# Kernel tuning notes

Measured on AMD Instinct MI355X. Metric: run time of the kernel, lower is better.

The kernel has to match this reference:

```python
import jax, jax.numpy as jnp
import numpy as np

K = 1024
D = 256
BETA = 0.25


def setup_inputs() -> dict:
    key = jax.random.key(0)
    kx, kc = jax.random.split(key)
    x = jax.random.normal(kx, (64, 32, 32, D), dtype=jnp.float32)
    limit = 1.0 / K
    codebook = jax.random.uniform(kc, (K, D), dtype=jnp.float32, minval=-limit, maxval=limit)
    return {"x": x, "codebook": codebook}


def reference(x, codebook):
    flat = x.reshape(-1, D)                                   # [N, D]
    x2 = jnp.sum(jnp.square(flat), axis=1, keepdims=True)     # [N, 1]
    e2 = jnp.sum(jnp.square(codebook), axis=1)                # [K]
    sim = flat @ codebook.T                                   # [N, K]
    dist = x2 + e2 - 2.0 * sim                                # [N, K]
    idx = jnp.argmin(dist, axis=1)                            # [N]
    q = codebook[idx].reshape(x.shape)                        # [..., D]

    q_st = jax.lax.stop_gradient(q)
    x_st = jax.lax.stop_gradient(x)
    commit = jnp.mean(jnp.square(q_st - x))
    codebk = jnp.mean(jnp.square(q - x_st))
    loss = BETA * commit + codebk

    # code-usage statistics via histogram (equivalent to mean of one-hot)
    counts = jnp.zeros((K,), dtype=x.dtype).at[idx].add(1.0)
    probs = counts / flat.shape[0]
    eps = jnp.asarray(1e-10, dtype=x.dtype)
    H = -jnp.sum(probs * jnp.log2(probs + eps))               # bits/index
    perplexity = jnp.exp(H * jnp.log(jnp.asarray(2.0, dtype=x.dtype)))
    usage = jnp.sum((probs > 0).astype(x.dtype)) / float(K)

    y = x + jax.lax.stop_gradient(q - x)                      # straight-through
    return y, idx, loss, perplexity, usage, H
```

## Files before the change

### kernel.cpp

```cpp
#include <hip/hip_runtime.h>
#include <math.h>

#define D       256
#define KCODES  1024
#define NROWS   65536
#define BETA    0.25f
#define MARGIN  1e-3f
#define MAXSURV 7

typedef __attribute__((ext_vector_type(8))) short bf16x8;
typedef __attribute__((ext_vector_type(4))) float f32x4;

__device__ __forceinline__ unsigned int bf16_rne(float f) {
    unsigned int u = __float_as_uint(f);
    return (u + 0x7FFFu + ((u >> 16) & 1u)) >> 16;
}
__device__ __forceinline__ f32x4 mfma16(bf16x8 a, bf16x8 b, f32x4 c) {
    return __builtin_amdgcn_mfma_f32_16x16x32_bf16(a, b, c, 0, 0, 0);
}

__global__ __launch_bounds__(256) void split_cb_kernel(const float* __restrict__ cb,
                                                       ushort* __restrict__ cs,
                                                       float* __restrict__ e2f) {
    int code = blockIdx.x * 4 + (threadIdx.x >> 6);
    int lane = threadIdx.x & 63;
    float4 v = ((const float4*)(cb + (size_t)code * D))[lane];
    double s = (double)v.x * v.x + (double)v.y * v.y +
               (double)v.z * v.z + (double)v.w * v.w;
    ushort* ph = cs + (size_t)code * 256 + lane * 4;
    ph[0] = (ushort)bf16_rne(v.x); ph[1] = (ushort)bf16_rne(v.y);
    ph[2] = (ushort)bf16_rne(v.z); ph[3] = (ushort)bf16_rne(v.w);
    #pragma unroll
    for (int off = 32; off > 0; off >>= 1) s += __shfl_down(s, off, 64);
    if (lane == 0) e2f[code] = (float)s;
}

__global__ __launch_bounds__(256, 1) void screen_kernel(
    const float* __restrict__ x, const ushort* __restrict__ cs,
    const float* __restrict__ e2f, float* __restrict__ x2f,
    ushort* __restrict__ rowlist)
{
    __shared__ __attribute__((aligned(16))) ushort Bt[2][32 * 264];
    unsigned* mrg = (unsigned*)&Bt[0][0];
    #define MRG(r, j) mrg[(r) * 33 + (j)]

    const int tid  = threadIdx.x;
    const int wave = tid >> 6, lane = tid & 63;
    const int quad = lane >> 4, m = lane & 15;
    const int rowBase = blockIdx.x * 256;
    const int wrb = rowBase + wave * 64;

    const int sc = tid & 31, sp = tid >> 5;
    bf16x8 stg[4];
    {
        const ushort* src = cs + (size_t)sc * 256 + sp * 32;
        #pragma unroll
        for (int i = 0; i < 4; ++i) stg[i] = *(const bf16x8*)&src[i * 8];
    }

    bf16x8 af[4][8];
    #pragma unroll
    for (int t = 0; t < 4; ++t) {
        const float* xr = x + (size_t)(wrb + t * 16 + m) * D;
        double s = 0.0;
        #pragma unroll
        for (int c = 0; c < 8; ++c) {
            float4 f0 = *(const float4*)&xr[c * 32 + quad * 8];
            float4 f1 = *(const float4*)&xr[c * 32 + quad * 8 + 4];
            s += (double)f0.x * f0.x + (double)f0.y * f0.y +
                 (double)f0.z * f0.z + (double)f0.w * f0.w;
            s += (double)f1.x * f1.x + (double)f1.y * f1.y +
                 (double)f1.z * f1.z + (double)f1.w * f1.w;
            float ff[8] = {f0.x, f0.y, f0.z, f0.w, f1.x, f1.y, f1.z, f1.w};
            #pragma unroll
            for (int j = 0; j < 8; ++j) af[t][c][j] = (short)bf16_rne(ff[j]);
        }
        s += __shfl_xor(s, 16, 64);
        s += __shfl_xor(s, 32, 64);
        if (quad == 0) x2f[wrb + t * 16 + m] = (float)s;
    }

    unsigned u1[4][4], u2[4][4];
    #pragma unroll
    for (int t = 0; t < 4; ++t)
        #pragma unroll
        for (int r = 0; r < 4; ++r) { u1[t][r] = 0xFFFFFFFFu; u2[t][r] = 0xFFFFFFFFu; }

    for (int kt = 0; kt < KCODES / 32; ++kt) {
        {
            ushort* dst = &Bt[kt & 1][sc * 264 + sp * 32];
            #pragma unroll
            for (int i = 0; i < 4; ++i) *(bf16x8*)&dst[i * 8] = stg[i];
        }
        __syncthreads();
        if (kt < KCODES / 32 - 1) {
            const ushort* src = cs + (size_t)((kt + 1) * 32 + sc) * 256 + sp * 32;
            #pragma unroll
            for (int i = 0; i < 4; ++i) stg[i] = *(const bf16x8*)&src[i * 8];
        }

        float e2pa = e2f[kt * 32 + m] + 0.5f;
        float e2pb = e2f[kt * 32 + 16 + m] + 0.5f;

        const ushort* Bcur = &Bt[kt & 1][0];
        #pragma unroll
        for (int nt = 0; nt < 2; ++nt) {
            f32x4 acc0 = {0.f, 0.f, 0.f, 0.f};
            f32x4 acc1 = {0.f, 0.f, 0.f, 0.f};
            f32x4 acc2 = {0.f, 0.f, 0.f, 0.f};
            f32x4 acc3 = {0.f, 0.f, 0.f, 0.f};
            const ushort* bp = Bcur + (nt * 16 + m) * 264 + quad * 8;
            __builtin_amdgcn_s_setprio(1);
            #pragma unroll
            for (int c = 0; c < 8; ++c) {
                bf16x8 bh = *(const bf16x8*)&bp[c * 32];
                acc0 = mfma16(af[0][c], bh, acc0);
                acc1 = mfma16(af[1][c], bh, acc1);
                acc2 = mfma16(af[2][c], bh, acc2);
                acc3 = mfma16(af[3][c], bh, acc3);
            }
            __builtin_amdgcn_s_setprio(0);
            unsigned kcode = kt * 32 + nt * 16 + m;
            float e2p = nt ? e2pb : e2pa;
            #pragma unroll
            for (int t = 0; t < 4; ++t) {
                f32x4 acc = (t == 0) ? acc0 : (t == 1) ? acc1 : (t == 2) ? acc2 : acc3;
                #pragma unroll
                for (int r = 0; r < 4; ++r) {
                    float d = fmaf(-2.f, acc[r], e2p);
                    unsigned u = (__float_as_uint(d) & 0xFFFFFC00u) | kcode;
                    bool lt1 = u < u1[t][r];
                    bool lt2 = u < u2[t][r];
                    u2[t][r] = lt2 ? (lt1 ? u1[t][r] : u) : u2[t][r];
                    u1[t][r] = lt1 ? u : u1[t][r];
                }
            }
        }
    }

    #pragma unroll
    for (int ph = 0; ph < 2; ++ph) {
        if ((wave >> 1) == ph) {
            #pragma unroll
            for (int t = 0; t < 4; ++t)
                #pragma unroll
                for (int r = 0; r < 4; ++r) {
                    int rowloc = (wave & 1) * 64 + t * 16 + quad * 4 + r;
                    MRG(rowloc, m * 2 + 0) = u1[t][r];
                    MRG(rowloc, m * 2 + 1) = u2[t][r];
                }
        }
        __syncthreads();
        if (tid < 128) {
            unsigned umin = 0xFFFFFFFFu;
            #pragma unroll
            for (int j = 0; j < 32; ++j) umin = min(umin, MRG(tid, j));
            float dfloor = __uint_as_float(umin & 0xFFFFFC00u);
            unsigned limu = (__float_as_uint(dfloor + MARGIN) & 0xFFFFFC00u) | 1023u;
            ushort out[8] = {0, 0, 0, 0, 0, 0, 0, 0};
            int cnt = 0;
            for (int j = 0; j < 32; ++j) {
                unsigned u = MRG(tid, j);
                if (u <= limu && cnt < MAXSURV) { out[1 + cnt] = (ushort)(u & 1023u); ++cnt; }
            }
            out[0] = (ushort)cnt;
            *(bf16x8*)&rowlist[(size_t)(rowBase + ph * 128 + tid) * 8] = *(bf16x8*)out;
        }
        __syncthreads();
    }
    #undef MRG
}

__global__ __launch_bounds__(256) void rescore_kernel(
    const float* __restrict__ x, const float* __restrict__ cb,
    const float* __restrict__ x2f, const float* __restrict__ e2f,
    const ushort* __restrict__ rowlist, float* __restrict__ out_idxf,
    unsigned int* __restrict__ counts, float* __restrict__ y,
    float* __restrict__ msepart)
{
    int row  = blockIdx.x * 4 + (threadIdx.x >> 6);
    int lane = threadIdx.x & 63;
    const ushort* lst = rowlist + (size_t)row * 8;
    int cnt = lst[0];
    float4 xv = ((const float4*)(x + (size_t)row * D))[lane];

    int bk;
    if (cnt == 1) {
        bk = lst[1];
    } else {
        float x2 = x2f[row];
        float bestd = 1e30f;
        int   bestk = 0;
        for (int s = 0; s < cnt; ++s) {
            int k = lst[1 + s];
            float4 cv = ((const float4*)(cb + (size_t)k * D))[lane];
            double p = (double)xv.x * cv.x + (double)xv.y * cv.y +
                       (double)xv.z * cv.z + (double)xv.w * cv.w;
            #pragma unroll
            for (int off = 32; off > 0; off >>= 1) p += __shfl_down(p, off, 64);
            float simf = (float)p;
            float tt   = x2 + e2f[k];
            float dq   = tt - 2.0f * simf;
            if (dq < bestd || (dq == bestd && k < bestk)) { bestd = dq; bestk = k; }
        }
        bk = __shfl(bestk, 0, 64);
    }
    if (lane == 0) {
        out_idxf[row] = (float)bk;
        atomicAdd(&counts[bk], 1u);
    }
    float4 q = ((const float4*)(cb + (size_t)bk * D))[lane];
    float4 dv;
    dv.x = q.x - xv.x; dv.y = q.y - xv.y; dv.z = q.z - xv.z; dv.w = q.w - xv.w;
    float4 yv;
    yv.x = xv.x + dv.x; yv.y = xv.y + dv.y; yv.z = xv.z + dv.z; yv.w = xv.w + dv.w;
    ((float4*)(y + (size_t)row * D))[lane] = yv;
    float s = dv.x * dv.x + dv.y * dv.y + dv.z * dv.z + dv.w * dv.w;
    #pragma unroll
    for (int off = 32; off > 0; off >>= 1) s += __shfl_down(s, off, 64);
    if (lane == 0) msepart[row] = s;
}

__global__ __launch_bounds__(1024) void stats_kernel(
    const unsigned int* __restrict__ counts, const float* __restrict__ msepart,
    float* __restrict__ outs)
{
    int t = threadIdx.x;
    float ms = 0.f;
    #pragma unroll
    for (int j = 0; j < 64; ++j) ms += msepart[t + 1024 * j];

    float p = (float)counts[t] * (1.0f / 65536.0f);
    float h = -p * log2f(p + 1e-10f);
    float u = (p > 0.f) ? 1.f : 0.f;
    #pragma unroll
    for (int off = 32; off > 0; off >>= 1) {
        h  += __shfl_down(h,  off, 64);
        u  += __shfl_down(u,  off, 64);
        ms += __shfl_down(ms, off, 64);
    }
    __shared__ float hs[16], us[16], mss[16];
    int lane = t & 63, w = t >> 6;
    if (lane == 0) { hs[w] = h; us[w] = u; mss[w] = ms; }
    __syncthreads();
    if (t == 0) {
        float H = 0.f, U = 0.f, M = 0.f;
        #pragma unroll
        for (int i = 0; i < 16; ++i) { H += hs[i]; U += us[i]; M += mss[i]; }
        float m = M * (1.0f / 16777216.0f);
        float loss = BETA * m + m;
        float perp = expf(H * 0.69314718055994530942f);
        outs[0] = loss;
        outs[1] = perp;
        outs[2] = U * (1.0f / 1024.0f);
        outs[3] = H;
    }
}

extern "C" void kernel_launch(void* const* d_in, const int* in_sizes, int n_in,
                              void* d_out, int out_size, void* d_ws, size_t ws_size,
                              hipStream_t stream) {
    const float* x  = (const float*)d_in[0];
    const float* cb = (const float*)d_in[1];
    float* out      = (float*)d_out;

    float* y        = out;
    float* out_idxf = out + 16777216;
    float* outs     = out + 16777216 + 65536;

    float*        x2f     = (float*)d_ws;
    float*        e2f     = (float*)((char*)d_ws + 262144);
    unsigned int* counts  = (unsigned int*)((char*)d_ws + 266240);
    ushort*       rowlist = (ushort*)((char*)d_ws + 270400);
    ushort*       cs      = (ushort*)((char*)d_ws + 1318976);
    float*        msepart = (float*)((char*)d_ws + 1843264);

    hipMemsetAsync((char*)d_ws + 266240, 0, 4096, stream);
    split_cb_kernel<<<KCODES / 4, 256, 0, stream>>>(cb, cs, e2f);
    screen_kernel<<<NROWS / 256, 256, 0, stream>>>(x, cs, e2f, x2f, rowlist);
    rescore_kernel<<<NROWS / 4, 256, 0, stream>>>(x, cb, x2f, e2f, rowlist,
                                                  out_idxf, counts, y, msepart);
    stats_kernel<<<1, 1024, 0, stream>>>(counts, msepart, outs);
}
```

Before: 221.5 us.

## Restructure screen kernel to 8 waves of 16 rows each for higher occupancy

The screen kernel changes from 256-thread blocks where each wave handles 64 rows (four 16-row MFMA tiles) to 512-thread blocks of 128 rows where each wave handles a single 16-row tile. Per-thread register use (A fragments, accumulators, top-2 trackers) drops about fourfold, so launch bounds allow up to four blocks per CU instead of one. The aim is more waves in flight to hide latency. In exchange, each codebook tile staged into LDS is reused across 4x fewer rows per wave, which raises LDS read traffic per MFMA and adds more barrier participants.

```diff
diff --git a/kernel.cpp b/kernel.cpp
--- a/kernel.cpp
+++ b/kernel.cpp
@@ -35,7 +35,7 @@
     if (lane == 0) e2f[code] = (float)s;
 }
 
-__global__ __launch_bounds__(256, 1) void screen_kernel(
+__global__ __launch_bounds__(512, 4) void screen_kernel(
     const float* __restrict__ x, const ushort* __restrict__ cs,
     const float* __restrict__ e2f, float* __restrict__ x2f,
     ushort* __restrict__ rowlist)
@@ -47,21 +47,20 @@
     const int tid  = threadIdx.x;
     const int wave = tid >> 6, lane = tid & 63;
     const int quad = lane >> 4, m = lane & 15;
-    const int rowBase = blockIdx.x * 256;
-    const int wrb = rowBase + wave * 64;
+    const int rowBase = blockIdx.x * 128;
+    const int wrb = rowBase + wave * 16;
 
     const int sc = tid & 31, sp = tid >> 5;
-    bf16x8 stg[4];
+    bf16x8 stg[2];
     {
-        const ushort* src = cs + (size_t)sc * 256 + sp * 32;
-        #pragma unroll
-        for (int i = 0; i < 4; ++i) stg[i] = *(const bf16x8*)&src[i * 8];
-    }
-
-    bf16x8 af[4][8];
-    #pragma unroll
-    for (int t = 0; t < 4; ++t) {
-        const float* xr = x + (size_t)(wrb + t * 16 + m) * D;
+        const ushort* src = cs + (size_t)sc * 256 + sp * 16;
+        stg[0] = *(const bf16x8*)&src[0];
+        stg[1] = *(const bf16x8*)&src[8];
+    }
+
+    bf16x8 af[8];
+    {
+        const float* xr = x + (size_t)(wrb + m) * D;
         double s = 0.0;
         #pragma unroll
         for (int c = 0; c < 8; ++c) {
@@ -73,30 +72,28 @@
                  (double)f1.z * f1.z + (double)f1.w * f1.w;
             float ff[8] = {f0.x, f0.y, f0.z, f0.w, f1.x, f1.y, f1.z, f1.w};
             #pragma unroll
-            for (int j = 0; j < 8; ++j) af[t][c][j] = (short)bf16_rne(ff[j]);
+            for (int j = 0; j < 8; ++j) af[c][j] = (short)bf16_rne(ff[j]);
         }
         s += __shfl_xor(s, 16, 64);
         s += __shfl_xor(s, 32, 64);
-        if (quad == 0) x2f[wrb + t * 16 + m] = (float)s;
-    }
-
-    unsigned u1[4][4], u2[4][4];
-    #pragma unroll
-    for (int t = 0; t < 4; ++t)
-        #pragma unroll
-        for (int r = 0; r < 4; ++r) { u1[t][r] = 0xFFFFFFFFu; u2[t][r] = 0xFFFFFFFFu; }
+        if (quad == 0) x2f[wrb + m] = (float)s;
+    }
+
+    unsigned u1[4], u2[4];
+    #pragma unroll
+    for (int r = 0; r < 4; ++r) { u1[r] = 0xFFFFFFFFu; u2[r] = 0xFFFFFFFFu; }
 
     for (int kt = 0; kt < KCODES / 32; ++kt) {
         {
-            ushort* dst = &Bt[kt & 1][sc * 264 + sp * 32];
-            #pragma unroll
-            for (int i = 0; i < 4; ++i) *(bf16x8*)&dst[i * 8] = stg[i];
+            ushort* dst = &Bt[kt & 1][sc * 264 + sp * 16];
+            *(bf16x8*)&dst[0] = stg[0];
+            *(bf16x8*)&dst[8] = stg[1];
         }
         __syncthreads();
         if (kt < KCODES / 32 - 1) {
-            const ushort* src = cs + (size_t)((kt + 1) * 32 + sc) * 256 + sp * 32;
-            #pragma unroll
-            for (int i = 0; i < 4; ++i) stg[i] = *(const bf16x8*)&src[i * 8];
+            const ushort* src = cs + (size_t)((kt + 1) * 32 + sc) * 256 + sp * 16;
+            stg[0] = *(const bf16x8*)&src[0];
+            stg[1] = *(const bf16x8*)&src[8];
         }
 
         float e2pa = e2f[kt * 32 + m] + 0.5f;
@@ -105,68 +102,50 @@
         const ushort* Bcur = &Bt[kt & 1][0];
         #pragma unroll
         for (int nt = 0; nt < 2; ++nt) {
-            f32x4 acc0 = {0.f, 0.f, 0.f, 0.f};
-            f32x4 acc1 = {0.f, 0.f, 0.f, 0.f};
-            f32x4 acc2 = {0.f, 0.f, 0.f, 0.f};
-            f32x4 acc3 = {0.f, 0.f, 0.f, 0.f};
+            f32x4 acc = {0.f, 0.f, 0.f, 0.f};
             const ushort* bp = Bcur + (nt * 16 + m) * 264 + quad * 8;
             __builtin_amdgcn_s_setprio(1);
             #pragma unroll
             for (int c = 0; c < 8; ++c) {
                 bf16x8 bh = *(const bf16x8*)&bp[c * 32];
-                acc0 = mfma16(af[0][c], bh, acc0);
-                acc1 = mfma16(af[1][c], bh, acc1);
-                acc2 = mfma16(af[2][c], bh, acc2);
-                acc3 = mfma16(af[3][c], bh, acc3);
+                acc = mfma16(af[c], bh, acc);
             }
             __builtin_amdgcn_s_setprio(0);
             unsigned kcode = kt * 32 + nt * 16 + m;
             float e2p = nt ? e2pb : e2pa;
             #pragma unroll
-            for (int t = 0; t < 4; ++t) {
-                f32x4 acc = (t == 0) ? acc0 : (t == 1) ? acc1 : (t == 2) ? acc2 : acc3;
-                #pragma unroll
-                for (int r = 0; r < 4; ++r) {
-                    float d = fmaf(-2.f, acc[r], e2p);
-                    unsigned u = (__float_as_uint(d) & 0xFFFFFC00u) | kcode;
-                    bool lt1 = u < u1[t][r];
-                    bool lt2 = u < u2[t][r];
-                    u2[t][r] = lt2 ? (lt1 ? u1[t][r] : u) : u2[t][r];
-                    u1[t][r] = lt1 ? u : u1[t][r];
-                }
+            for (int r = 0; r < 4; ++r) {
+                float d = fmaf(-2.f, acc[r], e2p);
+                unsigned u = (__float_as_uint(d) & 0xFFFFFC00u) | kcode;
+                bool lt1 = u < u1[r];
+                bool lt2 = u < u2[r];
+                u2[r] = lt2 ? (lt1 ? u1[r] : u) : u2[r];
+                u1[r] = lt1 ? u : u1[r];
             }
         }
     }
 
     #pragma unroll
-    for (int ph = 0; ph < 2; ++ph) {
-        if ((wave >> 1) == ph) {
-            #pragma unroll
-            for (int t = 0; t < 4; ++t)
-                #pragma unroll
-                for (int r = 0; r < 4; ++r) {
-                    int rowloc = (wave & 1) * 64 + t * 16 + quad * 4 + r;
-                    MRG(rowloc, m * 2 + 0) = u1[t][r];
-                    MRG(rowloc, m * 2 + 1) = u2[t][r];
-                }
-        }
-        __syncthreads();
-        if (tid < 128) {
-            unsigned umin = 0xFFFFFFFFu;
-            #pragma unroll
-            for (int j = 0; j < 32; ++j) umin = min(umin, MRG(tid, j));
-            float dfloor = __uint_as_float(umin & 0xFFFFFC00u);
-            unsigned limu = (__float_as_uint(dfloor + MARGIN) & 0xFFFFFC00u) | 1023u;
-            ushort out[8] = {0, 0, 0, 0, 0, 0, 0, 0};
-            int cnt = 0;
-            for (int j = 0; j < 32; ++j) {
-                unsigned u = MRG(tid, j);
-                if (u <= limu && cnt < MAXSURV) { out[1 + cnt] = (ushort)(u & 1023u); ++cnt; }
-            }
-            out[0] = (ushort)cnt;
-            *(bf16x8*)&rowlist[(size_t)(rowBase + ph * 128 + tid) * 8] = *(bf16x8*)out;
-        }
-        __syncthreads();
+    for (int r = 0; r < 4; ++r) {
+        int rowloc = wave * 16 + quad * 4 + r;
+        MRG(rowloc, m * 2 + 0) = u1[r];
+        MRG(rowloc, m * 2 + 1) = u2[r];
+    }
+    __syncthreads();
+    if (tid < 128) {
+        unsigned umin = 0xFFFFFFFFu;
+        #pragma unroll
+        for (int j = 0; j < 32; ++j) umin = min(umin, MRG(tid, j));
+        float dfloor = __uint_as_float(umin & 0xFFFFFC00u);
+        unsigned limu = (__float_as_uint(dfloor + MARGIN) & 0xFFFFFC00u) | 1023u;
+        ushort out[8] = {0, 0, 0, 0, 0, 0, 0, 0};
+        int cnt = 0;
+        for (int j = 0; j < 32; ++j) {
+            unsigned u = MRG(tid, j);
+            if (u <= limu && cnt < MAXSURV) { out[1 + cnt] = (ushort)(u & 1023u); ++cnt; }
+        }
+        out[0] = (ushort)cnt;
+        *(bf16x8*)&rowlist[(size_t)(rowBase + tid) * 8] = *(bf16x8*)out;
     }
     #undef MRG
 }
@@ -277,7 +256,7 @@
 
     hipMemsetAsync((char*)d_ws + 266240, 0, 4096, stream);
     split_cb_kernel<<<KCODES / 4, 256, 0, stream>>>(cb, cs, e2f);
-    screen_kernel<<<NROWS / 256, 256, 0, stream>>>(x, cs, e2f, x2f, rowlist);
+    screen_kernel<<<NROWS / 128, 512, 0, stream>>>(x, cs, e2f, x2f, rowlist);
     rescore_kernel<<<NROWS / 4, 256, 0, stream>>>(x, cb, x2f, e2f, rowlist,
                                                   out_idxf, counts, y, msepart);
     stats_kernel<<<1, 1024, 0, stream>>>(counts, msepart, outs);
```

Result: faster. 198.4 us (-10.4%).
